# Kernel optimization log

Measured on AMD Instinct MI355X. Metric: run time of the kernel, lower is better.

Reference implementation:

```python
import jax, jax.numpy as jnp
import numpy as np
from jax import lax

DIVISOR = 2.0


def setup_inputs() -> dict:
    key = jax.random.key(0)
    k1, k2, k3, k4 = jax.random.split(key, 4)
    B, Cin, D = 16, 8, 64
    Cout, K = 16, 3
    fan_in = Cin * K * K * K
    scale = 1.0 / np.sqrt(fan_in)
    x = jax.random.normal(k1, (B, Cin, D, D, D), dtype=jnp.float32)
    conv_weight = jax.random.normal(k2, (Cout, Cin, K, K, K), dtype=jnp.float32) * scale
    conv_bias = jax.random.normal(k3, (Cout,), dtype=jnp.float32) * scale
    bias = jax.random.normal(k4, (Cout, 1, 1, 1), dtype=jnp.float32) * 0.02
    return {"x": x, "conv_weight": conv_weight, "conv_bias": conv_bias, "bias": bias}


def reference(x, conv_weight, conv_bias, bias):
    # Conv3d, stride 1, no padding: (B,8,64,64,64) -> (B,16,62,62,62)
    y = lax.conv_general_dilated(
        x, conv_weight,
        window_strides=(1, 1, 1), padding='VALID',
        dimension_numbers=('NCDHW', 'OIDHW', 'NCDHW'))
    y = (y + conv_bias[None, :, None, None, None]) / DIVISOR
    # MaxPool3d kernel 2, stride 2: -> (B,16,31,31,31)
    y = lax.reduce_window(y, -jnp.inf, lax.max,
                          (1, 1, 2, 2, 2), (1, 1, 2, 2, 2), 'VALID')
    # AdaptiveAvgPool3d((1,1,1)) = mean over spatial dims
    y = jnp.mean(y, axis=(2, 3, 4), keepdims=True)  # (B,16,1,1,1)
    y = y + bias  # bias (16,1,1,1) broadcasts over batch
    # sum over channel dim (sum_dim=1, dim removed)
    return jnp.sum(y, axis=1)  # (B,1,1,1)
```

## Files before the change

### kernel.cpp

```cpp
#include <hip/hip_runtime.h>

#define NB    16
#define NCO   16
#define NCI   8
#define DIM   64
#define PDIM  31
#define NPOOL 29791.0f
#define NOFF  28
#define KGRP  7
#define WSCALE 16.0f

#define PHG_N   8
#define BLK_PER_B (PDIM * PHG_N)
#define TILE_CHUNKS (4*10*64)
#define LDS_CHUNKS  2576

typedef __attribute__((ext_vector_type(4))) float f32x4;

__device__ __forceinline__ float wave_reduce_sum(float v) {
#pragma unroll
    for (int off = 32; off > 0; off >>= 1)
        v += __shfl_down(v, off, 64);
    return v;
}

__device__ __forceinline__ unsigned int pack4_fp8(float a, float b, float c, float d) {
    int v = __builtin_amdgcn_cvt_pk_fp8_f32(a, b, 0, false);
    v = __builtin_amdgcn_cvt_pk_fp8_f32(c, d, v, true);
    return (unsigned int)v;
}

__global__ __launch_bounds__(512)
void wprep8_kernel(const float* __restrict__ w, long* __restrict__ wT)
{
    const int t = threadIdx.x;
    if (t >= NCO * NOFF) return;
    const int co  = t / NOFF;
    const int off = t % NOFF;
    float v[8];
#pragma unroll
    for (int ci = 0; ci < NCI; ++ci)
        v[ci] = (off < 27) ? w[(co * NCI + ci) * 27 + off] * (0.5f * WSCALE) : 0.0f;
    const unsigned int lo = pack4_fp8(v[0], v[1], v[2], v[3]);
    const unsigned int hi = pack4_fp8(v[4], v[5], v[6], v[7]);
    wT[t] = (long)(((unsigned long long)hi << 32) | lo);
}

__global__ __launch_bounds__(256, 4)
void conv_fused_kernel(const float* __restrict__ x,
                       const long* __restrict__ wT,
                       float* __restrict__ part)
{
    __shared__ __align__(16) unsigned long long lds8[LDS_CHUNKS];
    __shared__ float red[4];

    const int tid   = threadIdx.x;
    const int wave  = tid >> 6;
    const int lane  = tid & 63;
    const int nlane = lane & 15;
    const int o     = lane >> 4;

    const int phg = blockIdx.x;
    const int pd  = blockIdx.y;
    const int b   = blockIdx.z;
    const int oh0 = phg * 8;

    long wfrag[KGRP];
#pragma unroll
    for (int g = 0; g < KGRP; ++g)
        wfrag[g] = wT[nlane * NOFF + g * 4 + o];

    int delta[KGRP];
#pragma unroll
    for (int g = 0; g < KGRP; ++g) {
        int off = g * 4 + o;
        if (off >= 27) off = 0;
        const int kd = off / 9;
        const int r2 = off % 9;
        const int kh = r2 / 3;
        const int kw = r2 % 3;
        delta[g] = ((kd * 10 + kh) * 64 + kw) * 8;
    }

#pragma unroll 1
    for (int u = tid; u < 640; u += 256) {
        const int r  = u >> 4;
        const int q  = u & 15;
        const int dl = r / 10;
        const int hl = r - dl * 10;
        int h = oh0 + hl;
        h = (h > 63) ? 63 : h;
        const float* src = x + ((((size_t)b * NCI) * DIM + (2 * pd + dl)) * DIM + h) * DIM + q * 4;
        f32x4 v[8];
#pragma unroll
        for (int ci = 0; ci < NCI; ++ci)
            v[ci] = *reinterpret_cast<const f32x4*>(src + (size_t)ci * DIM * DIM * DIM);
        unsigned int ow[8];
#pragma unroll
        for (int j = 0; j < 4; ++j) {
            ow[2 * j]     = pack4_fp8(v[0][j], v[1][j], v[2][j], v[3][j]);
            ow[2 * j + 1] = pack4_fp8(v[4][j], v[5][j], v[6][j], v[7][j]);
        }
        uint4* dst = reinterpret_cast<uint4*>(&lds8[(size_t)r * 64 + q * 4]);
        dst[0] = make_uint4(ow[0], ow[1], ow[2], ow[3]);
        dst[1] = make_uint4(ow[4], ow[5], ow[6], ow[7]);
    }
    __syncthreads();

    float lsum = 0.0f;
    const int ph_global = phg * 4 + wave;
    if (ph_global < PDIM) {
        const char* ldsb = reinterpret_cast<const char*>(lds8);
#pragma unroll 1
        for (int owt = 0; owt < 4; ++owt) {
            int base_mt[4];
#pragma unroll
            for (int mt = 0; mt < 4; ++mt) {
                const int od_l = mt >> 1;
                const int oh_l = 2 * wave + (mt & 1);
                base_mt[mt] = ((od_l * 10 + oh_l) * 64 + owt * 16 + nlane) * 8;
            }
            f32x4 acc[4];
#pragma unroll
            for (int mt = 0; mt < 4; ++mt) acc[mt] = (f32x4){0.f, 0.f, 0.f, 0.f};

#pragma unroll
            for (int g = 0; g < KGRP; ++g) {
#pragma unroll
                for (int mt = 0; mt < 4; ++mt) {
                    const long bfrag = *reinterpret_cast<const long*>(
                        ldsb + base_mt[mt] + delta[g]);
                    acc[mt] = __builtin_amdgcn_mfma_f32_16x16x32_fp8_fp8(
                        wfrag[g], bfrag, acc[mt], 0, 0, 0);
                }
            }
            f32x4 mx;
#pragma unroll
            for (int r = 0; r < 4; ++r)
                mx[r] = fmaxf(fmaxf(acc[0][r], acc[1][r]), fmaxf(acc[2][r], acc[3][r]));
            float4 pooled;
            pooled.x = fmaxf(mx[0], __shfl_xor(mx[0], 1, 64));
            pooled.y = fmaxf(mx[1], __shfl_xor(mx[1], 1, 64));
            pooled.z = fmaxf(mx[2], __shfl_xor(mx[2], 1, 64));
            pooled.w = fmaxf(mx[3], __shfl_xor(mx[3], 1, 64));
            const int pw = owt * 8 + (nlane >> 1);
            if (((lane & 1) == 0) && (pw < PDIM))
                lsum += (pooled.x + pooled.y) + (pooled.z + pooled.w);
        }
    }

    const float v = wave_reduce_sum(lsum);
    if (lane == 0) red[wave] = v;
    __syncthreads();
    if (tid == 0)
        part[((size_t)b * PDIM + pd) * PHG_N + phg] = (red[0] + red[1]) + (red[2] + red[3]);
}

__global__ __launch_bounds__(256)
void finalize2_kernel(const float* __restrict__ part,
                      const float* __restrict__ cb,
                      const float* __restrict__ bias,
                      float* __restrict__ out)
{
    __shared__ float red[4];
    const int b = blockIdx.x;
    const int tid = threadIdx.x;
    float s = (tid < BLK_PER_B) ? part[(size_t)b * BLK_PER_B + tid] : 0.0f;
    s = wave_reduce_sum(s);
    if ((tid & 63) == 0) red[tid >> 6] = s;
    __syncthreads();
    if (tid == 0) {
        float bc = 0.0f;
#pragma unroll
        for (int c = 0; c < NCO; ++c) bc += 0.5f * cb[c] + bias[c];
        out[b] = (red[0] + red[1] + red[2] + red[3]) * (1.0f / (WSCALE * NPOOL)) + bc;
    }
}

#define SPATIAL (PDIM*PDIM)
#define NTILE 4

__global__ __launch_bounds__(256)
void conv_pool_fb_kernel(const float* __restrict__ x,
                         const float* __restrict__ w,
                         const float* __restrict__ cb,
                         float* __restrict__ part)
{
    __shared__ float w_s[NCI * 27];
    __shared__ float red[4];
    const int tid  = threadIdx.x;
    const int pd   = blockIdx.x >> 2;
    const int tile = blockIdx.x & 3;
    const int co   = blockIdx.y;
    const int b    = blockIdx.z;
    if (tid < NCI * 27) w_s[tid] = w[co * (NCI * 27) + tid];
    __syncthreads();
    const int s = tile * 256 + tid;
    const bool valid = (s < SPATIAL);
    const int ss = valid ? s : 0;
    const int ph = ss / PDIM;
    const int pw = ss - ph * PDIM;
    const int d0 = pd * 2, h0 = ph * 2, w0 = pw * 2;
    float acc[8];
#pragma unroll
    for (int i = 0; i < 8; ++i) acc[i] = 0.f;
    const float* xb = x + (size_t)b * NCI * DIM * DIM * DIM;
#pragma unroll 1
    for (int ci = 0; ci < NCI; ++ci) {
        float xin[4][4][4];
        const float* xc = xb + (size_t)ci * DIM * DIM * DIM;
#pragma unroll
        for (int dd = 0; dd < 4; ++dd)
#pragma unroll
            for (int hh = 0; hh < 4; ++hh) {
                const float* row = xc + ((d0 + dd) * DIM + (h0 + hh)) * DIM + w0;
                float2 a = *reinterpret_cast<const float2*>(row);
                float2 c = *reinterpret_cast<const float2*>(row + 2);
                xin[dd][hh][0] = a.x; xin[dd][hh][1] = a.y;
                xin[dd][hh][2] = c.x; xin[dd][hh][3] = c.y;
            }
        const float* wc = &w_s[ci * 27];
#pragma unroll
        for (int kd = 0; kd < 3; ++kd)
#pragma unroll
        for (int kh = 0; kh < 3; ++kh)
#pragma unroll
        for (int kw = 0; kw < 3; ++kw) {
            const float wt = wc[(kd * 3 + kh) * 3 + kw];
#pragma unroll
            for (int od = 0; od < 2; ++od)
#pragma unroll
            for (int oh = 0; oh < 2; ++oh)
#pragma unroll
            for (int ow2 = 0; ow2 < 2; ++ow2)
                acc[(od * 2 + oh) * 2 + ow2] += wt * xin[od + kd][oh + kh][ow2 + kw];
        }
    }
    float m = acc[0];
#pragma unroll
    for (int i = 1; i < 8; ++i) m = fmaxf(m, acc[i]);
    m = (m + cb[co]) * 0.5f;
    float contrib = valid ? m : 0.f;
    float v = wave_reduce_sum(contrib);
    if ((tid & 63) == 0) red[tid >> 6] = v;
    __syncthreads();
    if (tid == 0) atomicAdd(&part[b], red[0] + red[1] + red[2] + red[3]);
}

__global__ void zero_acc_kernel(float* __restrict__ part)
{
    if (threadIdx.x < NB) part[threadIdx.x] = 0.f;
}

__global__ void finalize_atomic_kernel(const float* __restrict__ part,
                                       const float* __restrict__ bias,
                                       float* __restrict__ out)
{
    const int t = threadIdx.x;
    if (t < NB) {
        float bs = 0.f;
#pragma unroll
        for (int c = 0; c < NCO; ++c) bs += bias[c];
        out[t] = part[t] * (1.0f / NPOOL) + bs;
    }
}

extern "C" void kernel_launch(void* const* d_in, const int* in_sizes, int n_in,
                              void* d_out, int out_size, void* d_ws, size_t ws_size,
                              hipStream_t stream) {
    const float* x    = (const float*)d_in[0];
    const float* w    = (const float*)d_in[1];
    const float* cb   = (const float*)d_in[2];
    const float* bias = (const float*)d_in[3];
    float* out = (float*)d_out;

    const size_t WT_BYTES  = (size_t)NCO * NOFF * 8;
    const size_t part_off  = 4096;
    const size_t needed    = part_off + (size_t)NB * BLK_PER_B * sizeof(float);

    if (ws_size >= needed) {
        char* wsb = (char*)d_ws;
        long*  wT  = (long*)wsb;
        float* prt = (float*)(wsb + part_off);

        wprep8_kernel<<<1, 512, 0, stream>>>(w, wT);
        conv_fused_kernel<<<dim3(PHG_N, PDIM, NB), 256, 0, stream>>>(x, wT, prt);
        finalize2_kernel<<<NB, 256, 0, stream>>>(prt, cb, bias, out);
        (void)WT_BYTES;
    } else {
        float* prt = (float*)d_ws;
        zero_acc_kernel<<<1, 64, 0, stream>>>(prt);
        dim3 grid(PDIM * NTILE, NCO, NB);
        conv_pool_fb_kernel<<<grid, 256, 0, stream>>>(x, w, cb, prt);
        finalize_atomic_kernel<<<1, 64, 0, stream>>>(prt, bias, out);
    }
}
```

Measured before the change: 42.77 us.

## Tile four pooled depth slices per block and fold weight prep into conv kernel

Each block now covers four pooled depth slices with a 10x10x64 LDS tile instead of one slice with a 4-deep tile. Adjacent slices share their halo rows, so less of x is loaded and converted to fp8 per output. The separate weight-prep kernel is removed: every block stages the fp32 weights in LDS and packs its own fp8 fragments. The finalize kernel becomes a single wave over 64 partials. In exchange, the larger LDS footprint lowers the occupancy target to 3 blocks, the grid shrinks to 1024 blocks, and every block repeats the weight packing.

```diff
diff --git a/kernel.cpp b/kernel.cpp
--- a/kernel.cpp
+++ b/kernel.cpp
@@ -11,9 +11,10 @@
 #define WSCALE 16.0f
 
 #define PHG_N   8
-#define BLK_PER_B (PDIM * PHG_N)
-#define TILE_CHUNKS (4*10*64)
-#define LDS_CHUNKS  2576
+#define PDC_N   8
+#define PARTS_PER_B (PHG_N * PDC_N)
+#define TILE_CHUNKS (10*10*64)
+#define LDS_CHUNKS  6408
 
 typedef __attribute__((ext_vector_type(4))) float f32x4;
 
@@ -30,25 +31,9 @@
     return (unsigned int)v;
 }
 
-__global__ __launch_bounds__(512)
-void wprep8_kernel(const float* __restrict__ w, long* __restrict__ wT)
-{
-    const int t = threadIdx.x;
-    if (t >= NCO * NOFF) return;
-    const int co  = t / NOFF;
-    const int off = t % NOFF;
-    float v[8];
-#pragma unroll
-    for (int ci = 0; ci < NCI; ++ci)
-        v[ci] = (off < 27) ? w[(co * NCI + ci) * 27 + off] * (0.5f * WSCALE) : 0.0f;
-    const unsigned int lo = pack4_fp8(v[0], v[1], v[2], v[3]);
-    const unsigned int hi = pack4_fp8(v[4], v[5], v[6], v[7]);
-    wT[t] = (long)(((unsigned long long)hi << 32) | lo);
-}
-
-__global__ __launch_bounds__(256, 4)
+__global__ __launch_bounds__(256, 3)
 void conv_fused_kernel(const float* __restrict__ x,
-                       const long* __restrict__ wT,
+                       const float* __restrict__ w,
                        float* __restrict__ part)
 {
     __shared__ __align__(16) unsigned long long lds8[LDS_CHUNKS];
@@ -61,14 +46,33 @@
     const int o     = lane >> 4;
 
     const int phg = blockIdx.x;
-    const int pd  = blockIdx.y;
+    const int pdc = blockIdx.y;
     const int b   = blockIdx.z;
     const int oh0 = phg * 8;
-
+    const int d0  = pdc * 8;
+
+    {
+        float* wl = reinterpret_cast<float*>(lds8);
+#pragma unroll 1
+        for (int i = tid; i < NCO * NCI * 27; i += 256) wl[i] = w[i];
+    }
+    __syncthreads();
     long wfrag[KGRP];
-#pragma unroll
-    for (int g = 0; g < KGRP; ++g)
-        wfrag[g] = wT[nlane * NOFF + g * 4 + o];
+    {
+        const float* wl = reinterpret_cast<const float*>(lds8);
+#pragma unroll
+        for (int g = 0; g < KGRP; ++g) {
+            const int off = g * 4 + o;
+            float v[8];
+#pragma unroll
+            for (int ci = 0; ci < NCI; ++ci)
+                v[ci] = (off < 27) ? wl[(nlane * NCI + ci) * 27 + off] * (0.5f * WSCALE) : 0.0f;
+            const unsigned int lo = pack4_fp8(v[0], v[1], v[2], v[3]);
+            const unsigned int hi = pack4_fp8(v[4], v[5], v[6], v[7]);
+            wfrag[g] = (long)(((unsigned long long)hi << 32) | lo);
+        }
+    }
+    __syncthreads();
 
     int delta[KGRP];
 #pragma unroll
@@ -83,14 +87,14 @@
     }
 
 #pragma unroll 1
-    for (int u = tid; u < 640; u += 256) {
+    for (int u = tid; u < 1600; u += 256) {
         const int r  = u >> 4;
         const int q  = u & 15;
         const int dl = r / 10;
         const int hl = r - dl * 10;
-        int h = oh0 + hl;
-        h = (h > 63) ? 63 : h;
-        const float* src = x + ((((size_t)b * NCI) * DIM + (2 * pd + dl)) * DIM + h) * DIM + q * 4;
+        int d = d0 + dl;  d = (d > 63) ? 63 : d;
+        int h = oh0 + hl; h = (h > 63) ? 63 : h;
+        const float* src = x + ((((size_t)b * NCI) * DIM + d) * DIM + h) * DIM + q * 4;
         f32x4 v[8];
 #pragma unroll
         for (int ci = 0; ci < NCI; ++ci)
@@ -112,40 +116,45 @@
     if (ph_global < PDIM) {
         const char* ldsb = reinterpret_cast<const char*>(lds8);
 #pragma unroll 1
-        for (int owt = 0; owt < 4; ++owt) {
-            int base_mt[4];
-#pragma unroll
-            for (int mt = 0; mt < 4; ++mt) {
-                const int od_l = mt >> 1;
-                const int oh_l = 2 * wave + (mt & 1);
-                base_mt[mt] = ((od_l * 10 + oh_l) * 64 + owt * 16 + nlane) * 8;
+        for (int pdl = 0; pdl < 4; ++pdl) {
+            const int pd = pdc * 4 + pdl;
+            if (pd >= PDIM) break;
+#pragma unroll 1
+            for (int owt = 0; owt < 4; ++owt) {
+                int base_mt[4];
+#pragma unroll
+                for (int mt = 0; mt < 4; ++mt) {
+                    const int od_l = mt >> 1;
+                    const int oh_l = 2 * wave + (mt & 1);
+                    base_mt[mt] = (((2 * pdl + od_l) * 10 + oh_l) * 64 + owt * 16 + nlane) * 8;
+                }
+                f32x4 acc[4];
+#pragma unroll
+                for (int mt = 0; mt < 4; ++mt) acc[mt] = (f32x4){0.f, 0.f, 0.f, 0.f};
+
+#pragma unroll
+                for (int g = 0; g < KGRP; ++g) {
+#pragma unroll
+                    for (int mt = 0; mt < 4; ++mt) {
+                        const long bfrag = *reinterpret_cast<const long*>(
+                            ldsb + base_mt[mt] + delta[g]);
+                        acc[mt] = __builtin_amdgcn_mfma_f32_16x16x32_fp8_fp8(
+                            wfrag[g], bfrag, acc[mt], 0, 0, 0);
+                    }
+                }
+                f32x4 mx;
+#pragma unroll
+                for (int r = 0; r < 4; ++r)
+                    mx[r] = fmaxf(fmaxf(acc[0][r], acc[1][r]), fmaxf(acc[2][r], acc[3][r]));
+                float4 pooled;
+                pooled.x = fmaxf(mx[0], __shfl_xor(mx[0], 1, 64));
+                pooled.y = fmaxf(mx[1], __shfl_xor(mx[1], 1, 64));
+                pooled.z = fmaxf(mx[2], __shfl_xor(mx[2], 1, 64));
+                pooled.w = fmaxf(mx[3], __shfl_xor(mx[3], 1, 64));
+                const int pw = owt * 8 + (nlane >> 1);
+                if (((lane & 1) == 0) && (pw < PDIM))
+                    lsum += (pooled.x + pooled.y) + (pooled.z + pooled.w);
             }
-            f32x4 acc[4];
-#pragma unroll
-            for (int mt = 0; mt < 4; ++mt) acc[mt] = (f32x4){0.f, 0.f, 0.f, 0.f};
-
-#pragma unroll
-            for (int g = 0; g < KGRP; ++g) {
-#pragma unroll
-                for (int mt = 0; mt < 4; ++mt) {
-                    const long bfrag = *reinterpret_cast<const long*>(
-                        ldsb + base_mt[mt] + delta[g]);
-                    acc[mt] = __builtin_amdgcn_mfma_f32_16x16x32_fp8_fp8(
-                        wfrag[g], bfrag, acc[mt], 0, 0, 0);
-                }
-            }
-            f32x4 mx;
-#pragma unroll
-            for (int r = 0; r < 4; ++r)
-                mx[r] = fmaxf(fmaxf(acc[0][r], acc[1][r]), fmaxf(acc[2][r], acc[3][r]));
-            float4 pooled;
-            pooled.x = fmaxf(mx[0], __shfl_xor(mx[0], 1, 64));
-            pooled.y = fmaxf(mx[1], __shfl_xor(mx[1], 1, 64));
-            pooled.z = fmaxf(mx[2], __shfl_xor(mx[2], 1, 64));
-            pooled.w = fmaxf(mx[3], __shfl_xor(mx[3], 1, 64));
-            const int pw = owt * 8 + (nlane >> 1);
-            if (((lane & 1) == 0) && (pw < PDIM))
-                lsum += (pooled.x + pooled.y) + (pooled.z + pooled.w);
         }
     }
 
@@ -153,27 +162,24 @@
     if (lane == 0) red[wave] = v;
     __syncthreads();
     if (tid == 0)
-        part[((size_t)b * PDIM + pd) * PHG_N + phg] = (red[0] + red[1]) + (red[2] + red[3]);
-}
-
-__global__ __launch_bounds__(256)
-void finalize2_kernel(const float* __restrict__ part,
+        part[((size_t)b * PHG_N + phg) * PDC_N + pdc] = (red[0] + red[1]) + (red[2] + red[3]);
+}
+
+__global__ __launch_bounds__(64)
+void finalize3_kernel(const float* __restrict__ part,
                       const float* __restrict__ cb,
                       const float* __restrict__ bias,
                       float* __restrict__ out)
 {
-    __shared__ float red[4];
-    const int b = blockIdx.x;
-    const int tid = threadIdx.x;
-    float s = (tid < BLK_PER_B) ? part[(size_t)b * BLK_PER_B + tid] : 0.0f;
+    const int b    = blockIdx.x;
+    const int lane = threadIdx.x;
+    float s = part[(size_t)b * PARTS_PER_B + lane];
     s = wave_reduce_sum(s);
-    if ((tid & 63) == 0) red[tid >> 6] = s;
-    __syncthreads();
-    if (tid == 0) {
+    if (lane == 0) {
         float bc = 0.0f;
 #pragma unroll
         for (int c = 0; c < NCO; ++c) bc += 0.5f * cb[c] + bias[c];
-        out[b] = (red[0] + red[1] + red[2] + red[3]) * (1.0f / (WSCALE * NPOOL)) + bc;
+        out[b] = s * (1.0f / (WSCALE * NPOOL)) + bc;
     }
 }
 
@@ -274,19 +280,12 @@
     const float* bias = (const float*)d_in[3];
     float* out = (float*)d_out;
 
-    const size_t WT_BYTES  = (size_t)NCO * NOFF * 8;
-    const size_t part_off  = 4096;
-    const size_t needed    = part_off + (size_t)NB * BLK_PER_B * sizeof(float);
+    const size_t needed = (size_t)NB * PARTS_PER_B * sizeof(float);
 
     if (ws_size >= needed) {
-        char* wsb = (char*)d_ws;
-        long*  wT  = (long*)wsb;
-        float* prt = (float*)(wsb + part_off);
-
-        wprep8_kernel<<<1, 512, 0, stream>>>(w, wT);
-        conv_fused_kernel<<<dim3(PHG_N, PDIM, NB), 256, 0, stream>>>(x, wT, prt);
-        finalize2_kernel<<<NB, 256, 0, stream>>>(prt, cb, bias, out);
-        (void)WT_BYTES;
+        float* prt = (float*)d_ws;
+        conv_fused_kernel<<<dim3(PHG_N, PDC_N, NB), 256, 0, stream>>>(x, w, prt);
+        finalize3_kernel<<<NB, 64, 0, stream>>>(prt, cb, bias, out);
     } else {
         float* prt = (float*)d_ws;
         zero_acc_kernel<<<1, 64, 0, stream>>>(prt);
```

Result: slower. 63.39 us (+48.2%).
